# Performance work log

Measured on AMD Instinct MI355X. Metric: run time of the kernel, lower is better.

The kernel has to match this reference:

```python
import jax, jax.numpy as jnp
import numpy as np

D_MODEL = 1024
NUM_HEADS = 16
HEAD_DIM = D_MODEL // NUM_HEADS
THETA = 10000.0
B, T = 2, 2048


def _init_w(key, d_out, d_in):
    std = np.sqrt(2.0 / (d_in + d_out))
    w = jax.random.truncated_normal(key, -3.0, 3.0, (d_out, d_in), dtype=jnp.float32)
    return w * std


def setup_inputs() -> dict:
    key = jax.random.key(0)
    k1, k2, k3, k4, k5, k6 = jax.random.split(key, 6)
    in_features = jax.random.normal(k1, (B, T, D_MODEL), dtype=jnp.float32)
    token_positions = jnp.sort(jax.random.randint(k2, (B, T), 0, T), axis=-1).astype(jnp.int32)
    Wq = _init_w(k3, D_MODEL, D_MODEL)
    Wk = _init_w(k4, D_MODEL, D_MODEL)
    Wv = _init_w(k5, D_MODEL, D_MODEL)
    Wo = _init_w(k6, D_MODEL, D_MODEL)
    return {"in_features": in_features, "token_positions": token_positions,
            "Wq": Wq, "Wk": Wk, "Wv": Wv, "Wo": Wo}


def _apply_rope(x, token_positions):
    # x: [B, H, T, hd]; token_positions: [B, T]
    hd = x.shape[-1]
    inv_freq = 1.0 / (THETA ** (2.0 * jnp.arange(hd // 2, dtype=jnp.float32) / hd))
    angles = token_positions[..., None].astype(jnp.float32) * inv_freq  # [B, T, hd/2]
    cos = jnp.cos(angles)[:, None, :, :]  # [B, 1, T, hd/2]
    sin = jnp.sin(angles)[:, None, :, :]
    xp = x.reshape(*x.shape[:-1], hd // 2, 2)  # interleaved pairs
    x0, x1 = xp[..., 0], xp[..., 1]
    out = jnp.stack([cos * x0 - sin * x1, cos * x1 + sin * x0], axis=-1)
    return out.reshape(x.shape)


def reference(in_features, token_positions, Wq, Wk, Wv, Wo):
    b, t, d = in_features.shape
    h, hd = NUM_HEADS, HEAD_DIM

    def proj(W):
        y = jnp.einsum('btd,ed->bte', in_features, W)
        return y.reshape(b, t, h, hd).transpose(0, 2, 1, 3)  # [B, H, T, hd]

    q, k, v = proj(Wq), proj(Wk), proj(Wv)
    q = _apply_rope(q, token_positions)
    k = _apply_rope(k, token_positions)

    scores = jnp.einsum('bhtd,bhsd->bhts', q, k) / jnp.sqrt(jnp.float32(hd))
    causal = jnp.tril(jnp.ones((t, t), dtype=bool))
    scores = jnp.where(causal, scores, -jnp.inf)
    attn = jax.nn.softmax(scores, axis=-1)
    out = jnp.einsum('bhts,bhsd->bhtd', attn, v)  # [B, H, T, hd]
    out = out.transpose(0, 2, 1, 3).reshape(b, t, d)
    return jnp.einsum('btd,ed->bte', out, Wo)
```

## Files before the change

kernel.cpp:

```cpp
#include <hip/hip_runtime.h>
#include <hip/hip_bf16.h>

#define BB 2
#define TT 2048
#define DM 1024
#define NH 16
#define HD 64
#define BT (BB*TT)
#define SC2 0.18033688011112042f

typedef unsigned short u16;
typedef __attribute__((ext_vector_type(8))) short short8;
typedef __attribute__((ext_vector_type(4))) float f32x4;

__device__ __forceinline__ u16 f2b(float f){
  unsigned u = __builtin_bit_cast(unsigned, f);
  u += 0x7FFFu + ((u >> 16) & 1u);
  return (u16)(u >> 16);
}
__device__ __forceinline__ float b2f(u16 h){
  unsigned u = ((unsigned)h) << 16;
  return __builtin_bit_cast(float, u);
}

__device__ __forceinline__ void gll16(const u16* g, u16* l){
  __builtin_amdgcn_global_load_lds((const __attribute__((address_space(1))) void*)g,
                                   (__attribute__((address_space(3))) void*)l, 16, 0, 0);
}

__global__ __launch_bounds__(256) void cvt_kernel(const float* __restrict__ src,
                                                  u16* __restrict__ dst, int n4){
  int i = blockIdx.x*256 + threadIdx.x;
  if (i < n4){
    const float4 v = *(const float4*)(src + (size_t)i*4);
    ushort4 o;
    o.x = f2b(v.x); o.y = f2b(v.y); o.z = f2b(v.z); o.w = f2b(v.w);
    *(ushort4*)(dst + (size_t)i*4) = o;
  }
}

__global__ __launch_bounds__(256) void cvt_w_kernel(const float* __restrict__ w0,
                                                    const float* __restrict__ w1,
                                                    const float* __restrict__ w2,
                                                    const float* __restrict__ w3,
                                                    u16* __restrict__ dst){
  const int seg = blockIdx.x >> 10;
  const int i = (blockIdx.x & 1023)*256 + threadIdx.x;
  const float* src = (seg==0)?w0:(seg==1)?w1:(seg==2)?w2:w3;
  const float4 v = *(const float4*)(src + (size_t)i*4);
  ushort4 o;
  o.x = f2b(v.x); o.y = f2b(v.y); o.z = f2b(v.z); o.w = f2b(v.w);
  *(ushort4*)(dst + (size_t)seg*DM*DM + (size_t)i*4) = o;
}

#define FRAG(buf, row) (*(const short8*)((buf) + (size_t)(row)*32 + ((g ^ (((row)>>1)&3))*8)))

template<int MODE>
__global__ __launch_bounds__(256) void gemm128(const u16* __restrict__ A,
                                               const u16* __restrict__ W,
                                               u16* __restrict__ Ybf,
                                               float* __restrict__ Yf){
  __shared__ u16 sA0[4096], sB0[4096], sA1[4096], sB1[4096];
  const int tid = threadIdx.x;
  const int lane = tid & 63;
  const int wave = tid >> 6;
  const int r = lane & 15, g = lane >> 4;
  const int wr = wave >> 1, wc = wave & 1;
  const int m0 = blockIdx.y << 7;
  const int nn0 = blockIdx.x << 7;

  const int srow = tid >> 2;
  const int lcol = (((tid & 3) ^ ((srow >> 1) & 3))) * 8;

  const u16* gA0 = A + (size_t)(m0 + srow)*DM + lcol;
  const u16* gA1 = gA0 + (size_t)64*DM;
  const u16* gB0 = W + (size_t)(nn0 + srow)*DM + lcol;
  const u16* gB1 = gB0 + (size_t)64*DM;

  f32x4 acc[4][4];
  #pragma unroll
  for (int i=0;i<4;i++)
    #pragma unroll
    for (int j=0;j<4;j++) acc[i][j] = (f32x4){0.f,0.f,0.f,0.f};

#define STAGE(SA, SB, koff) { \
    gll16(gA0 + (koff), SA + (size_t)tid*8); \
    gll16(gA1 + (koff), SA + 2048 + (size_t)tid*8); \
    gll16(gB0 + (koff), SB + (size_t)tid*8); \
    gll16(gB1 + (koff), SB + 2048 + (size_t)tid*8); }

#define COMPUTE(SA, SB) { \
    short8 af[4], bf[4]; \
    _Pragma("unroll") \
    for (int f=0; f<4; f++){ \
      af[f] = FRAG(SA, wr*64 + f*16 + r); \
      bf[f] = FRAG(SB, wc*64 + f*16 + r); \
    } \
    _Pragma("unroll") \
    for (int fr=0; fr<4; fr++) \
      _Pragma("unroll") \
      for (int fn=0; fn<4; fn++) \
        acc[fr][fn] = __builtin_amdgcn_mfma_f32_16x16x32_bf16(af[fr], bf[fn], acc[fr][fn], 0,0,0); }

  STAGE(sA0, sB0, 0);
  __syncthreads();

  for (int t = 0; t < 32; t += 2){
    if (t + 1 < 32) STAGE(sA1, sB1, (t+1)*32);
    COMPUTE(sA0, sB0);
    __syncthreads();
    if (t + 2 < 32) STAGE(sA0, sB0, (t+2)*32);
    COMPUTE(sA1, sB1);
    __syncthreads();
  }

  #pragma unroll
  for (int fr=0; fr<4; fr++){
    #pragma unroll
    for (int i=0;i<4;i++){
      const int m = m0 + wr*64 + fr*16 + g*4 + i;
      #pragma unroll
      for (int fn=0; fn<4; fn++){
        const int nn = nn0 + wc*64 + fn*16 + r;
        if (MODE == 0){
          Ybf[(size_t)(nn >> 10)*BT*DM + (size_t)m*DM + (nn & 1023)] = f2b(acc[fr][fn][i]);
        } else {
          Yf[(size_t)m*DM + nn] = acc[fr][fn][i];
        }
      }
    }
  }
#undef STAGE
#undef COMPUTE
}

__global__ __launch_bounds__(256) void rope_kernel(u16* __restrict__ Qb, u16* __restrict__ Kb,
                                                   const int* __restrict__ pos){
  const int t = blockIdx.x*256 + threadIdx.x;
  const int m = t >> 5;
  const int fi = t & 31;
  const float invf = __expf(-(float)fi * 0.28782313662425575f);
  float s, c;
  sincosf((float)pos[m] * invf, &s, &c);
  const float cq = c*SC2, sq = s*SC2;
  const size_t base = (size_t)m*DM + fi*2;
  #pragma unroll
  for (int h=0; h<NH; h++){
    const size_t a = base + h*HD;
    {
      const float x0 = b2f(Qb[a]), x1 = b2f(Qb[a+1]);
      Qb[a]   = f2b(cq*x0 - sq*x1);
      Qb[a+1] = f2b(cq*x1 + sq*x0);
    }
    {
      const float x0 = b2f(Kb[a]), x1 = b2f(Kb[a+1]);
      Kb[a]   = f2b(c*x0 - s*x1);
      Kb[a+1] = f2b(c*x1 + s*x0);
    }
  }
}

__global__ __launch_bounds__(256) void transpose_v_kernel(const u16* __restrict__ Vb,
                                                          u16* __restrict__ Vt){
  __shared__ u16 tile[64][72];
  const int bh = blockIdx.x >> 5;
  const int sc = blockIdx.x & 31;
  const int bq = bh >> 4, h = bh & 15;
  const int s0 = sc*64;
  {
    const int row = threadIdx.x >> 3;
    const int c8 = (threadIdx.x & 7)*8;
    #pragma unroll
    for (int rr = 0; rr < 64; rr += 32){
      const short8 v = *(const short8*)(Vb + (size_t)(bq*TT + s0 + row + rr)*DM + h*HD + c8);
      *(short8*)(&tile[row+rr][c8]) = v;
    }
  }
  __syncthreads();
  {
    const int d = threadIdx.x >> 3;
    const int s8 = (threadIdx.x & 7)*8;
    #pragma unroll
    for (int dd = 0; dd < 64; dd += 32){
      short8 ov;
      #pragma unroll
      for (int j=0;j<8;j++){
        const int sl = s8 + j;
        const int w = sl & 31;
        const int slog = (sl & 32) + (w >> 1) + ((w & 1) << 4);
        ov[j] = (short)tile[slog][d+dd];
      }
      *(short8*)(Vt + ((size_t)bh*HD + d + dd)*TT + s0 + s8) = ov;
    }
  }
}

template<bool MASKED>
__device__ __forceinline__ void proc_fast(
    const short8 qf0, const short8 qf1,
    const short8 k00, const short8 k01, const short8 k10, const short8 k11,
    const short8 v0, const short8 v1, const short8 v2, const short8 v3,
    f32x4& o0, f32x4& o1, f32x4& o2, f32x4& o3,
    float (&lsum)[4],
    const int q0, const int s0, const int r, const int g,
    u16 (*pbuf)[40])
{
  f32x4 sa0={0,0,0,0}, sa1={0,0,0,0};
  __builtin_amdgcn_s_setprio(1);
  sa0 = __builtin_amdgcn_mfma_f32_16x16x32_bf16(qf0, k00, sa0, 0,0,0);
  sa0 = __builtin_amdgcn_mfma_f32_16x16x32_bf16(qf1, k01, sa0, 0,0,0);
  sa1 = __builtin_amdgcn_mfma_f32_16x16x32_bf16(qf0, k10, sa1, 0,0,0);
  sa1 = __builtin_amdgcn_mfma_f32_16x16x32_bf16(qf1, k11, sa1, 0,0,0);
  __builtin_amdgcn_s_setprio(0);
  #pragma unroll
  for (int i=0;i<4;i++){
    float a = sa0[i], b = sa1[i];
    if (MASKED){
      const int q = q0 + g*4 + i;
      a = (s0 + r      <= q) ? a : -3.0e38f;
      b = (s0 + 16 + r <= q) ? b : -3.0e38f;
    }
    const float p0 = exp2f(a);
    const float p1 = exp2f(b);
    lsum[i] += p0 + p1;
    unsigned w;
    asm("v_cvt_pk_bf16_f32 %0, %1, %2" : "=v"(w) : "v"(p0), "v"(p1));
    *(unsigned*)(&pbuf[g*4+i][r*2]) = w;
  }
  const short8 pf = *(const short8*)(&pbuf[r][g*8]);
  __builtin_amdgcn_s_setprio(1);
  o0 = __builtin_amdgcn_mfma_f32_16x16x32_bf16(pf, v0, o0, 0,0,0);
  o1 = __builtin_amdgcn_mfma_f32_16x16x32_bf16(pf, v1, o1, 0,0,0);
  o2 = __builtin_amdgcn_mfma_f32_16x16x32_bf16(pf, v2, o2, 0,0,0);
  o3 = __builtin_amdgcn_mfma_f32_16x16x32_bf16(pf, v3, o3, 0,0,0);
  __builtin_amdgcn_s_setprio(0);
}

__global__ __launch_bounds__(256) void attn_kernel(const u16* __restrict__ Qb,
                                                   const u16* __restrict__ Kb,
                                                   const u16* __restrict__ Vt,
                                                   u16* __restrict__ Ob){
  __shared__ u16 Ks[2][4096];
  __shared__ u16 Vs[2][4096];
  __shared__ u16 Plds[4][16][40];
  const int tid = threadIdx.x;
  const int lane = tid & 63;
  const int wave = tid >> 6;
  const int r = lane & 15, g = lane >> 4;

  const int pp = blockIdx.x;
  const int bh = blockIdx.y;
  const int bq = bh >> 4, h = bh & 15;
  const int lo = pp, hi = 31 - pp;
  const int w0A = lo*64 + wave*16;
  const int w0B = hi*64 + wave*16;
  const int sAd = (w0A >> 5) << 5;
  const int sBd = (w0B >> 5) << 5;
  const int nb = hi + 1;

  const u16* QrowA = Qb + (size_t)(bq*TT + w0A + r)*DM + h*HD;
  const u16* QrowB = Qb + (size_t)(bq*TT + w0B + r)*DM + h*HD;
  const short8 qA0 = *(const short8*)(QrowA + g*8);
  const short8 qA1 = *(const short8*)(QrowA + 32 + g*8);
  const short8 qB0 = *(const short8*)(QrowB + g*8);
  const short8 qB1 = *(const short8*)(QrowB + 32 + g*8);

  const int srow = tid >> 3;
  const int scol = ((tid & 7) ^ (srow & 7)) * 8;
  const u16* Ksrc = Kb + (size_t)(bq*TT + srow)*DM + h*HD + scol;
  const u16* Vsrc = Vt + (size_t)bh*HD*TT + (size_t)srow*TT + scol;

  f32x4 oA0={0,0,0,0}, oA1={0,0,0,0}, oA2={0,0,0,0}, oA3={0,0,0,0};
  f32x4 oB0={0,0,0,0}, oB1={0,0,0,0}, oB2={0,0,0,0}, oB3={0,0,0,0};
  float lA[4] = {0.f,0.f,0.f,0.f}, lB[4] = {0.f,0.f,0.f,0.f};

#define STAGEKV(B, S64) { \
    gll16(Ksrc + (size_t)(S64)*DM,        Ks[B] + (size_t)tid*8); \
    gll16(Ksrc + (size_t)((S64)+32)*DM,   Ks[B] + 2048 + (size_t)tid*8); \
    gll16(Vsrc + (S64),                   Vs[B] + (size_t)tid*8); \
    gll16(Vsrc + (size_t)32*TT + (S64),   Vs[B] + 2048 + (size_t)tid*8); }

  STAGEKV(0, 0);
  __syncthreads();

  for (int ib = 0; ib < nb; ib++){
    const int cur = ib & 1;
    if (ib + 1 < nb) STAGEKV(cur ^ 1, (ib + 1)*64);
    const u16* kb_ = Ks[cur];
    const u16* vb_ = Vs[cur];
    #pragma unroll
    for (int half = 0; half < 2; half++){
      const int s0 = ib*64 + half*32;
      if (s0 > sBd) continue;
      const int rb = half*32 + r;
      const int ph0 = (g ^ (r & 7))*8;
      const int ph1 = ((g + 4) ^ (r & 7))*8;
      const short8 k00 = *(const short8*)(kb_ + (size_t)rb*64 + ph0);
      const short8 k01 = *(const short8*)(kb_ + (size_t)rb*64 + ph1);
      const short8 k10 = *(const short8*)(kb_ + (size_t)(rb+16)*64 + ph0);
      const short8 k11 = *(const short8*)(kb_ + (size_t)(rb+16)*64 + ph1);
      const int vc = ((half*4 + g) ^ (r & 7))*8;
      const short8 v0 = *(const short8*)(vb_ + (size_t)(r     )*64 + vc);
      const short8 v1 = *(const short8*)(vb_ + (size_t)(16 + r)*64 + vc);
      const short8 v2 = *(const short8*)(vb_ + (size_t)(32 + r)*64 + vc);
      const short8 v3 = *(const short8*)(vb_ + (size_t)(48 + r)*64 + vc);
      if (s0 <= sAd){
        if (s0 == sAd) proc_fast<true >(qA0,qA1,k00,k01,k10,k11,v0,v1,v2,v3,
                                        oA0,oA1,oA2,oA3,lA,w0A,s0,r,g,Plds[wave]);
        else           proc_fast<false>(qA0,qA1,k00,k01,k10,k11,v0,v1,v2,v3,
                                        oA0,oA1,oA2,oA3,lA,w0A,s0,r,g,Plds[wave]);
      }
      if (s0 == sBd) proc_fast<true >(qB0,qB1,k00,k01,k10,k11,v0,v1,v2,v3,
                                      oB0,oB1,oB2,oB3,lB,w0B,s0,r,g,Plds[wave]);
      else           proc_fast<false>(qB0,qB1,k00,k01,k10,k11,v0,v1,v2,v3,
                                      oB0,oB1,oB2,oB3,lB,w0B,s0,r,g,Plds[wave]);
    }
    __syncthreads();
  }
#undef STAGEKV

  #pragma unroll
  for (int off=8; off>0; off>>=1){
    #pragma unroll
    for (int i=0;i<4;i++){
      lA[i] += __shfl_xor(lA[i], off);
      lB[i] += __shfl_xor(lB[i], off);
    }
  }
  float invA[4], invB[4];
  #pragma unroll
  for (int i=0;i<4;i++){ invA[i] = 1.0f/lA[i]; invB[i] = 1.0f/lB[i]; }
  #pragma unroll
  for (int i=0;i<4;i++){
    const size_t rowA = (size_t)(bq*TT + w0A + g*4 + i)*DM + h*HD;
    Ob[rowA + r]      = f2b(oA0[i]*invA[i]);
    Ob[rowA + 16 + r] = f2b(oA1[i]*invA[i]);
    Ob[rowA + 32 + r] = f2b(oA2[i]*invA[i]);
    Ob[rowA + 48 + r] = f2b(oA3[i]*invA[i]);
    const size_t rowB = (size_t)(bq*TT + w0B + g*4 + i)*DM + h*HD;
    Ob[rowB + r]      = f2b(oB0[i]*invB[i]);
    Ob[rowB + 16 + r] = f2b(oB1[i]*invB[i]);
    Ob[rowB + 32 + r] = f2b(oB2[i]*invB[i]);
    Ob[rowB + 48 + r] = f2b(oB3[i]*invB[i]);
  }
}

extern "C" void kernel_launch(void* const* d_in, const int* in_sizes, int n_in,
                              void* d_out, int out_size, void* d_ws, size_t ws_size,
                              hipStream_t stream) {
  const float* X  = (const float*)d_in[0];
  const int* pos  = (const int*)d_in[1];
  const float* Wq = (const float*)d_in[2];
  const float* Wk = (const float*)d_in[3];
  const float* Wv = (const float*)d_in[4];
  const float* Wo = (const float*)d_in[5];
  float* out = (float*)d_out;

  char* ws = (char*)d_ws;
  u16* Xb = (u16*)ws;
  u16* Vt = (u16*)ws;
  u16* Wb = (u16*)(ws + (size_t)8*1024*1024);
  u16* Qb = (u16*)(ws + (size_t)16*1024*1024);
  u16* Kb = Qb + (size_t)BT*DM;
  u16* Vb = Kb + (size_t)BT*DM;
  u16* Ob = (u16*)(ws + (size_t)40*1024*1024);

  const int DD = DM*DM;
  cvt_kernel<<<4096, 256, 0, stream>>>(X, Xb, BT*DM/4);
  cvt_w_kernel<<<4096, 256, 0, stream>>>(Wq, Wk, Wv, Wo, Wb);

  gemm128<0><<<dim3(24, 32), 256, 0, stream>>>(Xb, Wb, Qb, nullptr);
  rope_kernel<<<512, 256, 0, stream>>>(Qb, Kb, pos);
  transpose_v_kernel<<<1024, 256, 0, stream>>>(Vb, Vt);
  attn_kernel<<<dim3(16, 32), 256, 0, stream>>>(Qb, Kb, Vt, Ob);
  gemm128<1><<<dim3(8, 32), 256, 0, stream>>>(Ob, Wb + 3*DD, nullptr, out);
}
```

Measured before the change: 131.2 us.

## Split attention KV halves across two wave groups and merge conversion kernels

The attention kernel grows to 512 threads. Two groups of four waves each handle one 32-key half of every 64-key KV tile, and their partial outputs and row sums are combined through shared memory at the end. This doubles the waves working per block to hide latency and cut the serial per-tile work, at the cost of extra barriers and a reduction step. It also merges the X and weight bf16 conversion kernels into one launch to save launch overhead.

New measurement: 123.7 us. 1.06x faster.

```diff
diff --git a/kernel.cpp b/kernel.cpp
--- a/kernel.cpp
+++ b/kernel.cpp
@@ -28,29 +28,30 @@
                                    (__attribute__((address_space(3))) void*)l, 16, 0, 0);
 }
 
-__global__ __launch_bounds__(256) void cvt_kernel(const float* __restrict__ src,
-                                                  u16* __restrict__ dst, int n4){
-  int i = blockIdx.x*256 + threadIdx.x;
-  if (i < n4){
-    const float4 v = *(const float4*)(src + (size_t)i*4);
-    ushort4 o;
-    o.x = f2b(v.x); o.y = f2b(v.y); o.z = f2b(v.z); o.w = f2b(v.w);
-    *(ushort4*)(dst + (size_t)i*4) = o;
-  }
-}
-
-__global__ __launch_bounds__(256) void cvt_w_kernel(const float* __restrict__ w0,
-                                                    const float* __restrict__ w1,
-                                                    const float* __restrict__ w2,
-                                                    const float* __restrict__ w3,
-                                                    u16* __restrict__ dst){
-  const int seg = blockIdx.x >> 10;
-  const int i = (blockIdx.x & 1023)*256 + threadIdx.x;
-  const float* src = (seg==0)?w0:(seg==1)?w1:(seg==2)?w2:w3;
+__global__ __launch_bounds__(256) void cvt_all_kernel(const float* __restrict__ X,
+                                                      const float* __restrict__ w0,
+                                                      const float* __restrict__ w1,
+                                                      const float* __restrict__ w2,
+                                                      const float* __restrict__ w3,
+                                                      u16* __restrict__ Xb,
+                                                      u16* __restrict__ Wb){
+  const int b = blockIdx.x;
+  const float* src;
+  u16* dst;
+  int i;
+  if (b < 4096){
+    src = X; dst = Xb; i = b*256 + threadIdx.x;
+  } else {
+    const int bb = b - 4096;
+    const int seg = bb >> 10;
+    src = (seg==0)?w0:(seg==1)?w1:(seg==2)?w2:w3;
+    dst = Wb + (size_t)seg*DM*DM;
+    i = (bb & 1023)*256 + threadIdx.x;
+  }
   const float4 v = *(const float4*)(src + (size_t)i*4);
   ushort4 o;
   o.x = f2b(v.x); o.y = f2b(v.y); o.z = f2b(v.z); o.w = f2b(v.w);
-  *(ushort4*)(dst + (size_t)seg*DM*DM + (size_t)i*4) = o;
+  *(ushort4*)(dst + (size_t)i*4) = o;
 }
 
 #define FRAG(buf, row) (*(const short8*)((buf) + (size_t)(row)*32 + ((g ^ (((row)>>1)&3))*8)))
@@ -236,24 +237,25 @@
   __builtin_amdgcn_s_setprio(0);
 }
 
-__global__ __launch_bounds__(256) void attn_kernel(const u16* __restrict__ Qb,
+__global__ __launch_bounds__(512) void attn_kernel(const u16* __restrict__ Qb,
                                                    const u16* __restrict__ Kb,
                                                    const u16* __restrict__ Vt,
                                                    u16* __restrict__ Ob){
-  __shared__ u16 Ks[2][4096];
-  __shared__ u16 Vs[2][4096];
-  __shared__ u16 Plds[4][16][40];
+  __shared__ u16 KVs[2][8192];
+  __shared__ u16 Plds[8][16][40];
   const int tid = threadIdx.x;
   const int lane = tid & 63;
   const int wave = tid >> 6;
+  const int wq = wave & 3;
+  const int par = wave >> 2;
   const int r = lane & 15, g = lane >> 4;
 
   const int pp = blockIdx.x;
   const int bh = blockIdx.y;
   const int bq = bh >> 4, h = bh & 15;
   const int lo = pp, hi = 31 - pp;
-  const int w0A = lo*64 + wave*16;
-  const int w0B = hi*64 + wave*16;
+  const int w0A = lo*64 + wq*16;
+  const int w0B = hi*64 + wq*16;
   const int sAd = (w0A >> 5) << 5;
   const int sBd = (w0B >> 5) << 5;
   const int nb = hi + 1;
@@ -275,10 +277,8 @@
   float lA[4] = {0.f,0.f,0.f,0.f}, lB[4] = {0.f,0.f,0.f,0.f};
 
 #define STAGEKV(B, S64) { \
-    gll16(Ksrc + (size_t)(S64)*DM,        Ks[B] + (size_t)tid*8); \
-    gll16(Ksrc + (size_t)((S64)+32)*DM,   Ks[B] + 2048 + (size_t)tid*8); \
-    gll16(Vsrc + (S64),                   Vs[B] + (size_t)tid*8); \
-    gll16(Vsrc + (size_t)32*TT + (S64),   Vs[B] + 2048 + (size_t)tid*8); }
+    gll16(Ksrc + (size_t)(S64)*DM, &KVs[B][0]    + (size_t)tid*8); \
+    gll16(Vsrc + (S64),            &KVs[B][4096] + (size_t)tid*8); }
 
   STAGEKV(0, 0);
   __syncthreads();
@@ -286,20 +286,18 @@
   for (int ib = 0; ib < nb; ib++){
     const int cur = ib & 1;
     if (ib + 1 < nb) STAGEKV(cur ^ 1, (ib + 1)*64);
-    const u16* kb_ = Ks[cur];
-    const u16* vb_ = Vs[cur];
-    #pragma unroll
-    for (int half = 0; half < 2; half++){
-      const int s0 = ib*64 + half*32;
-      if (s0 > sBd) continue;
-      const int rb = half*32 + r;
+    const int s0 = ib*64 + par*32;
+    if (s0 <= sBd){
+      const u16* kb_ = KVs[cur];
+      const u16* vb_ = KVs[cur] + 4096;
+      const int rb = par*32 + r;
       const int ph0 = (g ^ (r & 7))*8;
       const int ph1 = ((g + 4) ^ (r & 7))*8;
       const short8 k00 = *(const short8*)(kb_ + (size_t)rb*64 + ph0);
       const short8 k01 = *(const short8*)(kb_ + (size_t)rb*64 + ph1);
       const short8 k10 = *(const short8*)(kb_ + (size_t)(rb+16)*64 + ph0);
       const short8 k11 = *(const short8*)(kb_ + (size_t)(rb+16)*64 + ph1);
-      const int vc = ((half*4 + g) ^ (r & 7))*8;
+      const int vc = ((par*4 + g) ^ (r & 7))*8;
       const short8 v0 = *(const short8*)(vb_ + (size_t)(r     )*64 + vc);
       const short8 v1 = *(const short8*)(vb_ + (size_t)(16 + r)*64 + vc);
       const short8 v2 = *(const short8*)(vb_ + (size_t)(32 + r)*64 + vc);
@@ -319,29 +317,74 @@
   }
 #undef STAGEKV
 
-  #pragma unroll
-  for (int off=8; off>0; off>>=1){
-    #pragma unroll
-    for (int i=0;i<4;i++){
-      lA[i] += __shfl_xor(lA[i], off);
-      lB[i] += __shfl_xor(lB[i], off);
-    }
-  }
-  float invA[4], invB[4];
-  #pragma unroll
-  for (int i=0;i<4;i++){ invA[i] = 1.0f/lA[i]; invB[i] = 1.0f/lB[i]; }
-  #pragma unroll
-  for (int i=0;i<4;i++){
-    const size_t rowA = (size_t)(bq*TT + w0A + g*4 + i)*DM + h*HD;
-    Ob[rowA + r]      = f2b(oA0[i]*invA[i]);
-    Ob[rowA + 16 + r] = f2b(oA1[i]*invA[i]);
-    Ob[rowA + 32 + r] = f2b(oA2[i]*invA[i]);
-    Ob[rowA + 48 + r] = f2b(oA3[i]*invA[i]);
-    const size_t rowB = (size_t)(bq*TT + w0B + g*4 + i)*DM + h*HD;
-    Ob[rowB + r]      = f2b(oB0[i]*invB[i]);
-    Ob[rowB + 16 + r] = f2b(oB1[i]*invB[i]);
-    Ob[rowB + 32 + r] = f2b(oB2[i]*invB[i]);
-    Ob[rowB + 48 + r] = f2b(oB3[i]*invB[i]);
+  float* scr = (float*)&KVs[0][0];
+  const int mbase = wq*20*64 + lane;
+  if (par == 1){
+    #pragma unroll
+    for (int i=0;i<4;i++){
+      scr[mbase + (0*4+i)*64] = oA0[i];
+      scr[mbase + (1*4+i)*64] = oA1[i];
+      scr[mbase + (2*4+i)*64] = oA2[i];
+      scr[mbase + (3*4+i)*64] = oA3[i];
+      scr[mbase + (16+i)*64]  = lA[i];
+    }
+  }
+  __syncthreads();
+  if (par == 0){
+    #pragma unroll
+    for (int i=0;i<4;i++){
+      oA0[i] += scr[mbase + (0*4+i)*64];
+      oA1[i] += scr[mbase + (1*4+i)*64];
+      oA2[i] += scr[mbase + (2*4+i)*64];
+      oA3[i] += scr[mbase + (3*4+i)*64];
+      lA[i]  += scr[mbase + (16+i)*64];
+    }
+  }
+  __syncthreads();
+  if (par == 1){
+    #pragma unroll
+    for (int i=0;i<4;i++){
+      scr[mbase + (0*4+i)*64] = oB0[i];
+      scr[mbase + (1*4+i)*64] = oB1[i];
+      scr[mbase + (2*4+i)*64] = oB2[i];
+      scr[mbase + (3*4+i)*64] = oB3[i];
+      scr[mbase + (16+i)*64]  = lB[i];
+    }
+  }
+  __syncthreads();
+  if (par == 0){
+    #pragma unroll
+    for (int i=0;i<4;i++){
+      oB0[i] += scr[mbase + (0*4+i)*64];
+      oB1[i] += scr[mbase + (1*4+i)*64];
+      oB2[i] += scr[mbase + (2*4+i)*64];
+      oB3[i] += scr[mbase + (3*4+i)*64];
+      lB[i]  += scr[mbase + (16+i)*64];
+    }
+    #pragma unroll
+    for (int off=8; off>0; off>>=1){
+      #pragma unroll
+      for (int i=0;i<4;i++){
+        lA[i] += __shfl_xor(lA[i], off);
+        lB[i] += __shfl_xor(lB[i], off);
+      }
+    }
+    float invA[4], invB[4];
+    #pragma unroll
+    for (int i=0;i<4;i++){ invA[i] = 1.0f/lA[i]; invB[i] = 1.0f/lB[i]; }
+    #pragma unroll
+    for (int i=0;i<4;i++){
+      const size_t rowA = (size_t)(bq*TT + w0A + g*4 + i)*DM + h*HD;
+      Ob[rowA + r]      = f2b(oA0[i]*invA[i]);
+      Ob[rowA + 16 + r] = f2b(oA1[i]*invA[i]);
+      Ob[rowA + 32 + r] = f2b(oA2[i]*invA[i]);
+      Ob[rowA + 48 + r] = f2b(oA3[i]*invA[i]);
+      const size_t rowB = (size_t)(bq*TT + w0B + g*4 + i)*DM + h*HD;
+      Ob[rowB + r]      = f2b(oB0[i]*invB[i]);
+      Ob[rowB + 16 + r] = f2b(oB1[i]*invB[i]);
+      Ob[rowB + 32 + r] = f2b(oB2[i]*invB[i]);
+      Ob[rowB + 48 + r] = f2b(oB3[i]*invB[i]);
+    }
   }
 }
 
@@ -366,12 +409,11 @@
   u16* Ob = (u16*)(ws + (size_t)40*1024*1024);
 
   const int DD = DM*DM;
-  cvt_kernel<<<4096, 256, 0, stream>>>(X, Xb, BT*DM/4);
-  cvt_w_kernel<<<4096, 256, 0, stream>>>(Wq, Wk, Wv, Wo, Wb);
+  cvt_all_kernel<<<8192, 256, 0, stream>>>(X, Wq, Wk, Wv, Wo, Xb, Wb);
 
   gemm128<0><<<dim3(24, 32), 256, 0, stream>>>(Xb, Wb, Qb, nullptr);
   rope_kernel<<<512, 256, 0, stream>>>(Qb, Kb, pos);
   transpose_v_kernel<<<1024, 256, 0, stream>>>(Vb, Vt);
-  attn_kernel<<<dim3(16, 32), 256, 0, stream>>>(Qb, Kb, Vt, Ob);
+  attn_kernel<<<dim3(16, 32), 512, 0, stream>>>(Qb, Kb, Vt, Ob);
   gemm128<1><<<dim3(8, 32), 256, 0, stream>>>(Ob, Wb + 3*DD, nullptr, out);
 }
```
